# Performance work log

Measured on AMD Instinct MI355X. Metric: run time of the kernel, lower is better.

## Reference

```python
import jax, jax.numpy as jnp
import numpy as np

E = 4096      # num hyperedges (events)
H1 = 512      # hidden1
H2 = 128      # hidden2 (latent)
NA, NK, NV = 8192, 4096, 1024   # nodes per type: author / keyword / venue
NNZ = 131072  # nonzeros per incidence matrix
SCALE = 0.02  # weight init scale (keeps tanh/exp in sane range)


def setup_inputs() -> dict:
    key = jax.random.key(0)
    ks = iter(jax.random.split(key, 64))
    nrm = lambda shape, s=SCALE: jax.random.normal(next(ks), shape, jnp.float32) * s
    inp = {}
    for t, N in (("a", NA), ("k", NK), ("v", NV)):
        inp["rows_" + t] = jax.random.randint(next(ks), (NNZ,), 0, N, dtype=jnp.int32)
        inp["cols_" + t] = jax.random.randint(next(ks), (NNZ,), 0, E, dtype=jnp.int32)
        inp["vals_" + t] = jax.random.uniform(next(ks), (NNZ,), jnp.float32)
        inp["Wn_" + t] = nrm((E, H1));  inp["bn_" + t] = jnp.zeros((H1,), jnp.float32)
        inp["Wzm_" + t] = nrm((H1, H2)); inp["bzm_" + t] = jnp.zeros((H2,), jnp.float32)
        inp["Wzs_" + t] = nrm((H1, H2)); inp["bzs_" + t] = jnp.zeros((H2,), jnp.float32)
        inp["We_" + t] = nrm((N, H1));  inp["be_" + t] = jnp.zeros((H1,), jnp.float32)
        inp["eps_" + t] = jax.random.normal(next(ks), (N, H2), jnp.float32)
    inp["Watt"] = nrm((H1, H1 // 2)); inp["batt"] = jnp.zeros((H1 // 2,), jnp.float32)
    inp["uatt"] = nrm((H1 // 2,), 0.1)
    inp["Wem"] = nrm((H1, H2)); inp["bem"] = jnp.zeros((H2,), jnp.float32)
    inp["Wes"] = nrm((H1, H2)); inp["bes"] = jnp.zeros((H2,), jnp.float32)
    inp["eps_e"] = jax.random.normal(next(ks), (E, H2), jnp.float32)
    return inp


def _type_branch(rows, cols, vals, N, Wn, bn, Wzm, bzm, Wzs, bzs, We, be, eps):
    # node encoder: tanh(sparse_inc @ Wn + bn);  sparse_inc is [N, E] in COO form
    h = jnp.tanh(jax.ops.segment_sum(vals[:, None] * Wn[cols], rows, num_segments=N) + bn)
    zm = h @ Wzm + bzm
    zs = h @ Wzs + bzs
    z = zm + eps * jnp.exp(zs)          # reparameterization
    # edge encoder: tanh(sparse_inc^T @ We + be) -> [E, H1]
    e = jnp.tanh(jax.ops.segment_sum(vals[:, None] * We[rows], cols, num_segments=E) + be)
    return zm, z, e


def _forward(rows_a, cols_a, vals_a, Wn_a, bn_a, Wzm_a, bzm_a, Wzs_a, bzs_a, We_a, be_a, eps_a,
             rows_k, cols_k, vals_k, Wn_k, bn_k, Wzm_k, bzm_k, Wzs_k, bzs_k, We_k, be_k, eps_k,
             rows_v, cols_v, vals_v, Wn_v, bn_v, Wzm_v, bzm_v, Wzs_v, bzs_v, We_v, be_v, eps_v,
             Watt, batt, uatt, Wem, bem, Wes, bes, eps_e):
    zm_a, z_a, e_a = _type_branch(rows_a, cols_a, vals_a, NA, Wn_a, bn_a, Wzm_a, bzm_a, Wzs_a, bzs_a, We_a, be_a, eps_a)
    zm_k, z_k, e_k = _type_branch(rows_k, cols_k, vals_k, NK, Wn_k, bn_k, Wzm_k, bzm_k, Wzs_k, bzs_k, We_k, be_k, eps_k)
    zm_v, z_v, e_v = _type_branch(rows_v, cols_v, vals_v, NV, Wn_v, bn_v, Wzm_v, bzm_v, Wzs_v, bzs_v, We_v, be_v, eps_v)

    # HyperedgeAttention over node types: [E, T=3, H1]
    edge_embeds = jnp.stack([e_a, e_k, e_v], axis=1)
    u = jnp.tanh(jnp.einsum('eth,hd->etd', edge_embeds, Watt) + batt)
    scores = jnp.einsum('etd,d->et', u, uatt)
    alphas = jax.nn.softmax(scores, axis=1)                  # [E, T]
    edge_embed = jnp.einsum('et,eth->eh', alphas, edge_embeds)  # [E, H1]

    zem = edge_embed @ Wem + bem
    zes = edge_embed @ Wes + bes
    ze = zem + eps_e * jnp.exp(zes)

    # InnerDecoder: z_node @ z_edge^T per type, flattened (sampled and mean variants)
    recon = jnp.concatenate([
        (z_a @ ze.T).ravel(), (z_k @ ze.T).ravel(), (z_v @ ze.T).ravel(),
        (zm_a @ zem.T).ravel(), (zm_k @ zem.T).ravel(), (zm_v @ zem.T).ravel(),
    ])
    return recon


def reference(rows_a, cols_a, vals_a, rows_k, cols_k, vals_k, rows_v, cols_v, vals_v,
              Wn_a, bn_a, Wzm_a, bzm_a, Wzs_a, bzs_a, We_a, be_a, eps_a,
              Wn_k, bn_k, Wzm_k, bzm_k, Wzs_k, bzs_k, We_k, be_k, eps_k,
              Wn_v, bn_v, Wzm_v, bzm_v, Wzs_v, bzs_v, We_v, be_v, eps_v,
              Watt, batt, uatt, Wem, bem, Wes, bes, eps_e):
    return _forward(rows_a, cols_a, vals_a, Wn_a, bn_a, Wzm_a, bzm_a, Wzs_a, bzs_a, We_a, be_a, eps_a,
                    rows_k, cols_k, vals_k, Wn_k, bn_k, Wzm_k, bzm_k, Wzs_k, bzs_k, We_k, be_k, eps_k,
                    rows_v, cols_v, vals_v, Wn_v, bn_v, Wzm_v, bzm_v, Wzs_v, bzs_v, We_v, be_v, eps_v,
                    Watt, batt, uatt, Wem, bem, Wes, bes, eps_e)
```

## Files before the change

kernel.cpp:

```cpp
#include <hip/hip_runtime.h>
#include <hip/hip_bf16.h>

#define NE   4096
#define D1   512
#define D2   128
#define NNZV 131072
#define MTOT 13312

typedef __attribute__((ext_vector_type(8))) short bf16x8;
typedef __attribute__((ext_vector_type(4))) float f32x4;

struct Params {
  const int*   rows[3]; const int* cols[3]; const float* vals[3];
  const float* Wn[3];  const float* bn[3];
  const float* Wzm[3]; const float* bzm[3];
  const float* Wzs[3]; const float* bzs[3];
  const float* We[3];  const float* be[3];
  const float* eps[3];
  const float* Watt; const float* batt; const float* uatt;
  const float* Wem;  const float* bem;  const float* Wes; const float* bes;
  const float* eps_e;
  int* cnt[6]; int* ptr[6]; int* cur[6]; int2* spair[6];
  __hip_bfloat16* Wbf[6];
  __hip_bfloat16* hbf[3];
  __hip_bfloat16* ebf[3];
  __hip_bfloat16* eebf;
  __hip_bfloat16* Wzmt[3];
  __hip_bfloat16* Wzst[3];
  __hip_bfloat16* Wattt;
  __hip_bfloat16* Wemt;
  __hip_bfloat16* West;
  float* scores;
  __hip_bfloat16* Zbf; __hip_bfloat16* Zmbf; __hip_bfloat16* zebf; __hip_bfloat16* zembf;
  float* out;
  int rowbase[3];
  int n8pre[7];
  int ndw;
};

__device__ __forceinline__ float bf2f(short s) {
  return __uint_as_float((unsigned)(unsigned short)s << 16);
}

__device__ __forceinline__ int nseg_of(int sub) {
  if (sub & 1) return NE;
  int t = sub >> 1;
  return t == 0 ? 8192 : (t == 1 ? 4096 : 1024);
}

__global__ void prep_kernel(Params p) {
  int i = blockIdx.x * blockDim.x + threadIdx.x;
  if (i < p.ndw) { ((int*)p.cnt[0])[i] = 0; return; }
  int c = i - p.ndw;
  if (c < p.n8pre[6]) {
    int s = 0;
#pragma unroll
    for (int k = 1; k < 6; ++k) if (c >= p.n8pre[k]) s = k;
    int off8 = c - p.n8pre[s];
    int t = s >> 1;
    const float* src = (s & 1) ? p.We[t] : p.Wn[t];
    __hip_bfloat16* dst = p.Wbf[s];
    const float4 a = *(const float4*)&src[(size_t)off8 * 8];
    const float4 b = *(const float4*)&src[(size_t)off8 * 8 + 4];
    bf16x8 o;
    o[0] = (short)__bfloat16_as_ushort(__float2bfloat16(a.x));
    o[1] = (short)__bfloat16_as_ushort(__float2bfloat16(a.y));
    o[2] = (short)__bfloat16_as_ushort(__float2bfloat16(a.z));
    o[3] = (short)__bfloat16_as_ushort(__float2bfloat16(a.w));
    o[4] = (short)__bfloat16_as_ushort(__float2bfloat16(b.x));
    o[5] = (short)__bfloat16_as_ushort(__float2bfloat16(b.y));
    o[6] = (short)__bfloat16_as_ushort(__float2bfloat16(b.z));
    o[7] = (short)__bfloat16_as_ushort(__float2bfloat16(b.w));
    *(bf16x8*)&dst[(size_t)off8 * 8] = o;
    return;
  }
  int cz = c - p.n8pre[6];
  if (cz < 6 * D1 * D2) {
    int m = cz >> 16, e = cz & 65535;
    int t = m >> 1;
    const float* src = (m & 1) ? p.Wzs[t] : p.Wzm[t];
    __hip_bfloat16* dst = (m & 1) ? p.Wzst[t] : p.Wzmt[t];
    int k = e >> 7, n = e & 127;
    dst[n * D1 + k] = __float2bfloat16(src[e]);
    return;
  }
  int cz2 = cz - 6 * D1 * D2;
  if (cz2 < D1 * 256) {
    int k = cz2 >> 8, n = cz2 & 255;
    p.Wattt[n * D1 + k] = __float2bfloat16(p.Watt[(size_t)k * 256 + n]);
    return;
  }
  int cz3 = cz2 - D1 * 256;
  if (cz3 < 2 * D1 * D2) {
    int m = cz3 >> 16, e = cz3 & 65535;
    const float* src = m ? p.Wes : p.Wem;
    __hip_bfloat16* dst = m ? p.West : p.Wemt;
    int k = e >> 7, n = e & 127;
    dst[n * D1 + k] = __float2bfloat16(src[e]);
  }
}

__global__ void hist_kernel(Params p) {
  int i = blockIdx.x * blockDim.x + threadIdx.x;
  if (i >= 6 * NNZV) return;
  int sub = i >> 17, idx = i & (NNZV - 1);
  int type = sub >> 1, dir = sub & 1;
  int seg = dir ? p.cols[type][idx] : p.rows[type][idx];
  atomicAdd(&p.cnt[sub][seg], 1);
}

__global__ __launch_bounds__(1024) void scan_kernel(Params p) {
  int sub = blockIdx.x;
  int n = nseg_of(sub);
  const int* cnt = p.cnt[sub];
  int* ptr = p.ptr[sub];
  int* cur = p.cur[sub];
  __shared__ int lds[1024];
  int tid = threadIdx.x;
  int per = (n + 1023) >> 10;
  int base = tid * per;
  int s = 0;
  for (int q = 0; q < per; ++q) { int ix = base + q; if (ix < n) s += cnt[ix]; }
  lds[tid] = s;
  __syncthreads();
  for (int off = 1; off < 1024; off <<= 1) {
    int v = (tid >= off) ? lds[tid - off] : 0;
    __syncthreads();
    lds[tid] += v;
    __syncthreads();
  }
  int prefix = (tid == 0) ? 0 : lds[tid - 1];
  for (int q = 0; q < per; ++q) {
    int ix = base + q;
    if (ix < n) { int c = cnt[ix]; ptr[ix] = prefix; cur[ix] = prefix; prefix += c; }
  }
  if (tid == 1023) ptr[n] = lds[1023];
}

__global__ void scatter_kernel(Params p) {
  int i = blockIdx.x * blockDim.x + threadIdx.x;
  if (i >= 6 * NNZV) return;
  int sub = i >> 17, idx = i & (NNZV - 1);
  int type = sub >> 1, dir = sub & 1;
  int seg = dir ? p.cols[type][idx] : p.rows[type][idx];
  int oth = dir ? p.rows[type][idx] : p.cols[type][idx];
  int pos = atomicAdd(&p.cur[sub][seg], 1);
  p.spair[sub][pos] = make_int2(oth, __float_as_int(p.vals[type][idx]));
}

__global__ __launch_bounds__(128) void spmm_kernel(Params p) {
  int g = blockIdx.x * 2 + (threadIdx.x >> 6);
  int sub, seg;
  if      (g <  8192) { sub = 0; seg = g;         }
  else if (g < 12288) { sub = 1; seg = g - 8192;  }
  else if (g < 16384) { sub = 2; seg = g - 12288; }
  else if (g < 20480) { sub = 3; seg = g - 16384; }
  else if (g < 21504) { sub = 4; seg = g - 20480; }
  else                { sub = 5; seg = g - 21504; }
  int type = sub >> 1, dir = sub & 1;
  const __hip_bfloat16* W = p.Wbf[sub];
  const float* bias = dir ? p.be[type] : p.bn[type];
  const int*  ptr  = p.ptr[sub];
  const int2* pair = p.spair[sub];
  int lane = threadIdx.x & 63;
  int c0 = lane * 8;
  float acc[8];
#pragma unroll
  for (int j = 0; j < 8; ++j) acc[j] = 0.f;
  int q0 = ptr[seg], q1 = ptr[seg + 1];
  int q = q0;
  for (; q + 4 <= q1; q += 4) {
    int2 pr0 = pair[q], pr1 = pair[q + 1], pr2 = pair[q + 2], pr3 = pair[q + 3];
    const bf16x8 w0 = *(const bf16x8*)(W + (size_t)pr0.x * D1 + c0);
    const bf16x8 w1 = *(const bf16x8*)(W + (size_t)pr1.x * D1 + c0);
    const bf16x8 w2 = *(const bf16x8*)(W + (size_t)pr2.x * D1 + c0);
    const bf16x8 w3 = *(const bf16x8*)(W + (size_t)pr3.x * D1 + c0);
    float v0 = __int_as_float(pr0.y), v1 = __int_as_float(pr1.y);
    float v2 = __int_as_float(pr2.y), v3 = __int_as_float(pr3.y);
#pragma unroll
    for (int j = 0; j < 8; ++j)
      acc[j] += v0 * bf2f(w0[j]) + v1 * bf2f(w1[j]) + v2 * bf2f(w2[j]) + v3 * bf2f(w3[j]);
  }
  for (; q < q1; ++q) {
    int2 pr = pair[q];
    const bf16x8 wv = *(const bf16x8*)(W + (size_t)pr.x * D1 + c0);
    float v = __int_as_float(pr.y);
#pragma unroll
    for (int j = 0; j < 8; ++j) acc[j] += v * bf2f(wv[j]);
  }
  const float4 b0 = *(const float4*)&bias[c0];
  const float4 b1 = *(const float4*)&bias[c0 + 4];
  float r[8];
  r[0] = tanhf(acc[0] + b0.x); r[1] = tanhf(acc[1] + b0.y);
  r[2] = tanhf(acc[2] + b0.z); r[3] = tanhf(acc[3] + b0.w);
  r[4] = tanhf(acc[4] + b1.x); r[5] = tanhf(acc[5] + b1.y);
  r[6] = tanhf(acc[6] + b1.z); r[7] = tanhf(acc[7] + b1.w);
  bf16x8 ob;
#pragma unroll
  for (int j = 0; j < 8; ++j) ob[j] = (short)__bfloat16_as_ushort(__float2bfloat16(r[j]));
  __hip_bfloat16* outp = dir ? p.ebf[type] : p.hbf[type];
  *(bf16x8*)&outp[(size_t)seg * D1 + c0] = ob;
}

__global__ __launch_bounds__(256) void zmzs_scores_kernel(Params p) {
  int b = blockIdx.x;
  int wid = threadIdx.x >> 6, lane = threadIdx.x & 63;
  int rloc = lane & 15, kg = lane >> 4;
  f32x4 zero = {0.f, 0.f, 0.f, 0.f};
  if (b < 208) {
    int type, blk;
    if      (b < 128) { type = 0; blk = b;       }
    else if (b < 192) { type = 1; blk = b - 128; }
    else              { type = 2; blk = b - 192; }
    int row0 = blk * 64 + wid * 16;
    const __hip_bfloat16* A  = p.hbf[type];
    const __hip_bfloat16* Bm = p.Wzmt[type];
    const __hip_bfloat16* Bs = p.Wzst[type];
    int mrow = row0 + rloc;
    f32x4 accm[8], accs[8];
#pragma unroll
    for (int nf = 0; nf < 8; ++nf) { accm[nf] = zero; accs[nf] = zero; }
    for (int kk = 0; kk < 16; ++kk) {
      bf16x8 a = *(const bf16x8*)(A + (size_t)mrow * D1 + kk * 32 + kg * 8);
#pragma unroll
      for (int nf = 0; nf < 8; ++nf) {
        int ncol = nf * 16 + rloc;
        bf16x8 bm = *(const bf16x8*)(Bm + (size_t)ncol * D1 + kk * 32 + kg * 8);
        accm[nf] = __builtin_amdgcn_mfma_f32_16x16x32_bf16(a, bm, accm[nf], 0, 0, 0);
        bf16x8 bs = *(const bf16x8*)(Bs + (size_t)ncol * D1 + kk * 32 + kg * 8);
        accs[nf] = __builtin_amdgcn_mfma_f32_16x16x32_bf16(a, bs, accs[nf], 0, 0, 0);
      }
    }
    int base = p.rowbase[type];
    const float* eps = p.eps[type];
    const float* bzm = p.bzm[type];
    const float* bzs = p.bzs[type];
    int rbase = row0 + kg * 4;
#pragma unroll
    for (int nf = 0; nf < 8; ++nf) {
      int col = nf * 16 + rloc;
      float bm = bzm[col], bs = bzs[col];
#pragma unroll
      for (int jj = 0; jj < 4; ++jj) {
        int row = rbase + jj;
        float zm = accm[nf][jj] + bm;
        float zs = accs[nf][jj] + bs;
        float ep = eps[(size_t)row * D2 + col];
        float z  = zm + ep * expf(zs);
        size_t oi = (size_t)(base + row) * D2 + col;
        p.Zmbf[oi] = __float2bfloat16(zm);
        p.Zbf[oi]  = __float2bfloat16(z);
      }
    }
  } else {
    int wtile = (b - 208) * 4 + wid;
    int t = wtile >> 8;
    int tile = wtile & 255;
    const __hip_bfloat16* A = p.ebf[t];
    const __hip_bfloat16* B = p.Wattt;
    int mrow = tile * 16 + rloc;
    f32x4 acc[16];
#pragma unroll
    for (int nf = 0; nf < 16; ++nf) acc[nf] = zero;
    for (int kk = 0; kk < 16; ++kk) {
      bf16x8 a = *(const bf16x8*)(A + (size_t)mrow * D1 + kk * 32 + kg * 8);
#pragma unroll
      for (int nf = 0; nf < 16; ++nf) {
        int ncol = nf * 16 + rloc;
        bf16x8 bv = *(const bf16x8*)(B + (size_t)ncol * D1 + kk * 32 + kg * 8);
        acc[nf] = __builtin_amdgcn_mfma_f32_16x16x32_bf16(a, bv, acc[nf], 0, 0, 0);
      }
    }
    float part[4] = {0.f, 0.f, 0.f, 0.f};
#pragma unroll
    for (int nf = 0; nf < 16; ++nf) {
      int col = nf * 16 + rloc;
      float ua = p.uatt[col], ba = p.batt[col];
#pragma unroll
      for (int jj = 0; jj < 4; ++jj)
        part[jj] += ua * tanhf(acc[nf][jj] + ba);
    }
#pragma unroll
    for (int off = 1; off < 16; off <<= 1) {
#pragma unroll
      for (int jj = 0; jj < 4; ++jj)
        part[jj] += __shfl_xor(part[jj], off, 64);
    }
    if (rloc == 0) {
#pragma unroll
      for (int jj = 0; jj < 4; ++jj) {
        int e = tile * 16 + kg * 4 + jj;
        p.scores[e * 3 + t] = part[jj];
      }
    }
  }
}

__global__ __launch_bounds__(256) void combine_kernel(Params p) {
  int e = blockIdx.x * 4 + (threadIdx.x >> 6);
  int lane = threadIdx.x & 63;
  float s0 = p.scores[e * 3 + 0];
  float s1 = p.scores[e * 3 + 1];
  float s2 = p.scores[e * 3 + 2];
  float m = fmaxf(s0, fmaxf(s1, s2));
  float a0 = expf(s0 - m), a1 = expf(s1 - m), a2 = expf(s2 - m);
  float inv = 1.f / (a0 + a1 + a2);
  a0 *= inv; a1 *= inv; a2 *= inv;
  int c0 = lane * 8;
  const bf16x8 va = *(const bf16x8*)(p.ebf[0] + (size_t)e * D1 + c0);
  const bf16x8 vk = *(const bf16x8*)(p.ebf[1] + (size_t)e * D1 + c0);
  const bf16x8 vv = *(const bf16x8*)(p.ebf[2] + (size_t)e * D1 + c0);
  bf16x8 o;
#pragma unroll
  for (int j = 0; j < 8; ++j) {
    float v = a0 * bf2f(va[j]) + a1 * bf2f(vk[j]) + a2 * bf2f(vv[j]);
    o[j] = (short)__bfloat16_as_ushort(__float2bfloat16(v));
  }
  *(bf16x8*)&p.eebf[(size_t)e * D1 + c0] = o;
}

__global__ __launch_bounds__(256) void zemzs_kernel(Params p) {
  int wid = threadIdx.x >> 6, lane = threadIdx.x & 63;
  int rloc = lane & 15, kg = lane >> 4;
  int row0 = blockIdx.x * 32 + (wid >> 1) * 16;
  int nh = wid & 1;
  const __hip_bfloat16* A  = p.eebf;
  const __hip_bfloat16* Bm = p.Wemt;
  const __hip_bfloat16* Bs = p.West;
  int mrow = row0 + rloc;
  f32x4 accm[4], accs[4];
  f32x4 zero = {0.f, 0.f, 0.f, 0.f};
#pragma unroll
  for (int nf = 0; nf < 4; ++nf) { accm[nf] = zero; accs[nf] = zero; }
  for (int kk = 0; kk < 16; ++kk) {
    bf16x8 a = *(const bf16x8*)(A + (size_t)mrow * D1 + kk * 32 + kg * 8);
#pragma unroll
    for (int nf = 0; nf < 4; ++nf) {
      int ncol = nh * 64 + nf * 16 + rloc;
      bf16x8 bm = *(const bf16x8*)(Bm + (size_t)ncol * D1 + kk * 32 + kg * 8);
      accm[nf] = __builtin_amdgcn_mfma_f32_16x16x32_bf16(a, bm, accm[nf], 0, 0, 0);
      bf16x8 bs = *(const bf16x8*)(Bs + (size_t)ncol * D1 + kk * 32 + kg * 8);
      accs[nf] = __builtin_amdgcn_mfma_f32_16x16x32_bf16(a, bs, accs[nf], 0, 0, 0);
    }
  }
  int rbase = row0 + kg * 4;
#pragma unroll
  for (int nf = 0; nf < 4; ++nf) {
    int col = nh * 64 + nf * 16 + rloc;
    float bm = p.bem[col], bs = p.bes[col];
#pragma unroll
    for (int jj = 0; jj < 4; ++jj) {
      int row = rbase + jj;
      float zm = accm[nf][jj] + bm;
      float zs = accs[nf][jj] + bs;
      float ep = p.eps_e[(size_t)row * D2 + col];
      float z  = zm + ep * expf(zs);
      size_t oi = (size_t)row * D2 + col;
      p.zembf[oi] = __float2bfloat16(zm);
      p.zebf[oi]  = __float2bfloat16(z);
    }
  }
}

#define DT_N 128
__global__ __launch_bounds__(256) void decode_kernel(Params p) {
  __shared__ __align__(16) float cs[64][DT_N + 4];
  int which = blockIdx.z;
  const __hip_bfloat16* A = which ? p.Zmbf  : p.Zbf;
  const __hip_bfloat16* B = which ? p.zembf : p.zebf;
  float* C = p.out + (size_t)which * MTOT * NE;
  int n0 = blockIdx.x * DT_N;
  int m0 = blockIdx.y * 64;
  int wid  = threadIdx.x >> 6;
  int lane = threadIdx.x & 63;
  int rloc = lane & 15;
  int kg   = lane >> 4;
  int mrow = m0 + wid * 16 + rloc;
  bf16x8 a[4];
#pragma unroll
  for (int kk = 0; kk < 4; ++kk)
    a[kk] = *(const bf16x8*)(A + (size_t)mrow * D2 + kk * 32 + kg * 8);
  f32x4 acc[DT_N / 16];
  f32x4 zero = {0.f, 0.f, 0.f, 0.f};
#pragma unroll
  for (int nf = 0; nf < DT_N / 16; ++nf) acc[nf] = zero;
#pragma unroll
  for (int nf = 0; nf < DT_N / 16; ++nf) {
    int ncol = n0 + nf * 16 + rloc;
#pragma unroll
    for (int kk = 0; kk < 4; ++kk) {
      bf16x8 bv = *(const bf16x8*)(B + (size_t)ncol * D2 + kk * 32 + kg * 8);
      acc[nf] = __builtin_amdgcn_mfma_f32_16x16x32_bf16(a[kk], bv, acc[nf], 0, 0, 0);
    }
  }
#pragma unroll
  for (int nf = 0; nf < DT_N / 16; ++nf)
#pragma unroll
    for (int jj = 0; jj < 4; ++jj)
      cs[wid * 16 + kg * 4 + jj][nf * 16 + rloc] = acc[nf][jj];
  __syncthreads();
  int r_l  = threadIdx.x >> 5;
  int c4   = (threadIdx.x & 31) * 4;
#pragma unroll
  for (int it = 0; it < 8; ++it) {
    int r = it * 8 + r_l;
    f32x4 v = *(const f32x4*)&cs[r][c4];
    __builtin_nontemporal_store(v, (f32x4*)&C[(size_t)(m0 + r) * NE + n0 + c4]);
  }
}

extern "C" void kernel_launch(void* const* d_in, const int* in_sizes, int n_in,
                              void* d_out, int out_size, void* d_ws, size_t ws_size,
                              hipStream_t stream) {
  (void)in_sizes; (void)n_in; (void)out_size; (void)ws_size;
  static const int Ns[3] = {8192, 4096, 1024};
  static const int NsegH[6] = {8192, 4096, 4096, 4096, 1024, 4096};

  Params p;
  for (int t = 0; t < 3; ++t) {
    const int o = t * 12;
    p.rows[t] = (const int*)d_in[o + 0];
    p.cols[t] = (const int*)d_in[o + 1];
    p.vals[t] = (const float*)d_in[o + 2];
    p.Wn[t]   = (const float*)d_in[o + 3];
    p.bn[t]   = (const float*)d_in[o + 4];
    p.Wzm[t]  = (const float*)d_in[o + 5];
    p.bzm[t]  = (const float*)d_in[o + 6];
    p.Wzs[t]  = (const float*)d_in[o + 7];
    p.bzs[t]  = (const float*)d_in[o + 8];
    p.We[t]   = (const float*)d_in[o + 9];
    p.be[t]   = (const float*)d_in[o + 10];
    p.eps[t]  = (const float*)d_in[o + 11];
  }
  p.Watt  = (const float*)d_in[36];
  p.batt  = (const float*)d_in[37];
  p.uatt  = (const float*)d_in[38];
  p.Wem   = (const float*)d_in[39];
  p.bem   = (const float*)d_in[40];
  p.Wes   = (const float*)d_in[41];
  p.bes   = (const float*)d_in[42];
  p.eps_e = (const float*)d_in[43];
  p.out = (float*)d_out;
  p.rowbase[0] = 0; p.rowbase[1] = 8192; p.rowbase[2] = 12288;

  char* ws = (char*)d_ws;
  size_t off = 0;
  auto alloc = [&](size_t bytes) -> char* {
    char* r = ws + off;
    off += (bytes + 255) & ~(size_t)255;
    return r;
  };
  for (int s = 0; s < 6; ++s) p.cnt[s] = (int*)alloc((size_t)(NsegH[s] + 1) * 4);
  size_t cnt_bytes = off;
  for (int s = 0; s < 6; ++s) {
    p.ptr[s]   = (int*)alloc((size_t)(NsegH[s] + 1) * 4);
    p.cur[s]   = (int*)alloc((size_t)(NsegH[s] + 1) * 4);
    p.spair[s] = (int2*)alloc((size_t)NNZV * 8);
  }
  for (int s = 0; s < 6; ++s) {
    int t = s >> 1;
    int nrows = (s & 1) ? Ns[t] : NE;
    p.Wbf[s] = (__hip_bfloat16*)alloc((size_t)nrows * D1 * 2);
  }
  for (int t = 0; t < 3; ++t) p.hbf[t]  = (__hip_bfloat16*)alloc((size_t)Ns[t] * D1 * 2);
  for (int t = 0; t < 3; ++t) p.ebf[t]  = (__hip_bfloat16*)alloc((size_t)NE * D1 * 2);
  p.eebf = (__hip_bfloat16*)alloc((size_t)NE * D1 * 2);
  for (int t = 0; t < 3; ++t) p.Wzmt[t] = (__hip_bfloat16*)alloc((size_t)D2 * D1 * 2);
  for (int t = 0; t < 3; ++t) p.Wzst[t] = (__hip_bfloat16*)alloc((size_t)D2 * D1 * 2);
  p.Wattt = (__hip_bfloat16*)alloc((size_t)256 * D1 * 2);
  p.Wemt  = (__hip_bfloat16*)alloc((size_t)D2 * D1 * 2);
  p.West  = (__hip_bfloat16*)alloc((size_t)D2 * D1 * 2);
  p.scores = (float*)alloc((size_t)NE * 3 * 4);
  p.Zbf    = (__hip_bfloat16*)alloc((size_t)MTOT * D2 * 2);
  p.Zmbf   = (__hip_bfloat16*)alloc((size_t)MTOT * D2 * 2);
  p.zebf   = (__hip_bfloat16*)alloc((size_t)NE * D2 * 2);
  p.zembf  = (__hip_bfloat16*)alloc((size_t)NE * D2 * 2);

  p.ndw = (int)(cnt_bytes >> 2);
  p.n8pre[0] = 0;
  for (int s = 0; s < 6; ++s) {
    int t = s >> 1;
    int nrows = (s & 1) ? Ns[t] : NE;
    p.n8pre[s + 1] = p.n8pre[s] + nrows * (D1 / 8);
  }

  int prep_threads = p.ndw + p.n8pre[6] + 6 * D1 * D2 + D1 * 256 + 2 * D1 * D2;
  prep_kernel       <<<(prep_threads + 255) / 256, 256, 0, stream>>>(p);
  hist_kernel       <<<(6 * NNZV + 255) / 256, 256, 0, stream>>>(p);
  scan_kernel       <<<6, 1024, 0, stream>>>(p);
  scatter_kernel    <<<(6 * NNZV + 255) / 256, 256, 0, stream>>>(p);
  spmm_kernel       <<<12800, 128, 0, stream>>>(p);
  zmzs_scores_kernel<<<400, 256, 0, stream>>>(p);
  combine_kernel    <<<1024, 256, 0, stream>>>(p);
  zemzs_kernel      <<<128, 256, 0, stream>>>(p);
  decode_kernel     <<<dim3(NE / DT_N, 208, 2), 256, 0, stream>>>(p);
}
```

Baseline: 542.7 us.

## Fuse attention combine into zemzs GEMM and histogram into prep kernel

The softmax-weighted combine of the three edge embeddings now runs inside the zem/zes GEMM kernel. Each block builds its 32 combined rows in shared memory, so the eebf intermediate buffer and its global round trip go away. The histogram atomics move into the prep kernel, and a small zero kernel clears the counters beforehand, which removes one launch. The transposed weight conversions now iterate so that consecutive threads write contiguous destinations, which coalesces stores but strides the reads.

```diff
diff --git a/kernel.cpp b/kernel.cpp
--- a/kernel.cpp
+++ b/kernel.cpp
@@ -24,7 +24,6 @@
   __hip_bfloat16* Wbf[6];
   __hip_bfloat16* hbf[3];
   __hip_bfloat16* ebf[3];
-  __hip_bfloat16* eebf;
   __hip_bfloat16* Wzmt[3];
   __hip_bfloat16* Wzst[3];
   __hip_bfloat16* Wattt;
@@ -41,6 +40,9 @@
 __device__ __forceinline__ float bf2f(short s) {
   return __uint_as_float((unsigned)(unsigned short)s << 16);
 }
+__device__ __forceinline__ short f2bf(float f) {
+  return (short)__bfloat16_as_ushort(__float2bfloat16(f));
+}
 
 __device__ __forceinline__ int nseg_of(int sub) {
   if (sub & 1) return NE;
@@ -48,10 +50,21 @@
   return t == 0 ? 8192 : (t == 1 ? 4096 : 1024);
 }
 
+__global__ void zero_kernel(int* base, int ndw) {
+  int i = blockIdx.x * blockDim.x + threadIdx.x;
+  if (i < ndw) base[i] = 0;
+}
+
 __global__ void prep_kernel(Params p) {
   int i = blockIdx.x * blockDim.x + threadIdx.x;
-  if (i < p.ndw) { ((int*)p.cnt[0])[i] = 0; return; }
-  int c = i - p.ndw;
+  if (i < 6 * NNZV) {
+    int sub = i >> 17, idx = i & (NNZV - 1);
+    int type = sub >> 1, dir = sub & 1;
+    int seg = dir ? p.cols[type][idx] : p.rows[type][idx];
+    atomicAdd(&p.cnt[sub][seg], 1);
+    return;
+  }
+  int c = i - 6 * NNZV;
   if (c < p.n8pre[6]) {
     int s = 0;
 #pragma unroll
@@ -63,50 +76,35 @@
     const float4 a = *(const float4*)&src[(size_t)off8 * 8];
     const float4 b = *(const float4*)&src[(size_t)off8 * 8 + 4];
     bf16x8 o;
-    o[0] = (short)__bfloat16_as_ushort(__float2bfloat16(a.x));
-    o[1] = (short)__bfloat16_as_ushort(__float2bfloat16(a.y));
-    o[2] = (short)__bfloat16_as_ushort(__float2bfloat16(a.z));
-    o[3] = (short)__bfloat16_as_ushort(__float2bfloat16(a.w));
-    o[4] = (short)__bfloat16_as_ushort(__float2bfloat16(b.x));
-    o[5] = (short)__bfloat16_as_ushort(__float2bfloat16(b.y));
-    o[6] = (short)__bfloat16_as_ushort(__float2bfloat16(b.z));
-    o[7] = (short)__bfloat16_as_ushort(__float2bfloat16(b.w));
+    o[0] = f2bf(a.x); o[1] = f2bf(a.y); o[2] = f2bf(a.z); o[3] = f2bf(a.w);
+    o[4] = f2bf(b.x); o[5] = f2bf(b.y); o[6] = f2bf(b.z); o[7] = f2bf(b.w);
     *(bf16x8*)&dst[(size_t)off8 * 8] = o;
     return;
   }
   int cz = c - p.n8pre[6];
   if (cz < 6 * D1 * D2) {
-    int m = cz >> 16, e = cz & 65535;
+    int m = cz >> 16, e2 = cz & 65535;
     int t = m >> 1;
     const float* src = (m & 1) ? p.Wzs[t] : p.Wzm[t];
     __hip_bfloat16* dst = (m & 1) ? p.Wzst[t] : p.Wzmt[t];
-    int k = e >> 7, n = e & 127;
-    dst[n * D1 + k] = __float2bfloat16(src[e]);
+    int n = e2 >> 9, k = e2 & 511;
+    dst[n * D1 + k] = __float2bfloat16(src[(size_t)k * D2 + n]);
     return;
   }
   int cz2 = cz - 6 * D1 * D2;
   if (cz2 < D1 * 256) {
-    int k = cz2 >> 8, n = cz2 & 255;
+    int n = cz2 >> 9, k = cz2 & 511;
     p.Wattt[n * D1 + k] = __float2bfloat16(p.Watt[(size_t)k * 256 + n]);
     return;
   }
   int cz3 = cz2 - D1 * 256;
   if (cz3 < 2 * D1 * D2) {
-    int m = cz3 >> 16, e = cz3 & 65535;
+    int m = cz3 >> 16, e2 = cz3 & 65535;
     const float* src = m ? p.Wes : p.Wem;
     __hip_bfloat16* dst = m ? p.West : p.Wemt;
-    int k = e >> 7, n = e & 127;
-    dst[n * D1 + k] = __float2bfloat16(src[e]);
-  }
-}
-
-__global__ void hist_kernel(Params p) {
-  int i = blockIdx.x * blockDim.x + threadIdx.x;
-  if (i >= 6 * NNZV) return;
-  int sub = i >> 17, idx = i & (NNZV - 1);
-  int type = sub >> 1, dir = sub & 1;
-  int seg = dir ? p.cols[type][idx] : p.rows[type][idx];
-  atomicAdd(&p.cnt[sub][seg], 1);
+    int n = e2 >> 9, k = e2 & 511;
+    dst[n * D1 + k] = __float2bfloat16(src[(size_t)k * D2 + n]);
+  }
 }
 
 __global__ __launch_bounds__(1024) void scan_kernel(Params p) {
@@ -197,7 +195,7 @@
   r[6] = tanhf(acc[6] + b1.z); r[7] = tanhf(acc[7] + b1.w);
   bf16x8 ob;
 #pragma unroll
-  for (int j = 0; j < 8; ++j) ob[j] = (short)__bfloat16_as_ushort(__float2bfloat16(r[j]));
+  for (int j = 0; j < 8; ++j) ob[j] = f2bf(r[j]);
   __hip_bfloat16* outp = dir ? p.ebf[type] : p.hbf[type];
   *(bf16x8*)&outp[(size_t)seg * D1 + c0] = ob;
 }
@@ -296,44 +294,46 @@
   }
 }
 
-__global__ __launch_bounds__(256) void combine_kernel(Params p) {
-  int e = blockIdx.x * 4 + (threadIdx.x >> 6);
-  int lane = threadIdx.x & 63;
-  float s0 = p.scores[e * 3 + 0];
-  float s1 = p.scores[e * 3 + 1];
-  float s2 = p.scores[e * 3 + 2];
-  float m = fmaxf(s0, fmaxf(s1, s2));
-  float a0 = expf(s0 - m), a1 = expf(s1 - m), a2 = expf(s2 - m);
-  float inv = 1.f / (a0 + a1 + a2);
-  a0 *= inv; a1 *= inv; a2 *= inv;
-  int c0 = lane * 8;
-  const bf16x8 va = *(const bf16x8*)(p.ebf[0] + (size_t)e * D1 + c0);
-  const bf16x8 vk = *(const bf16x8*)(p.ebf[1] + (size_t)e * D1 + c0);
-  const bf16x8 vv = *(const bf16x8*)(p.ebf[2] + (size_t)e * D1 + c0);
-  bf16x8 o;
-#pragma unroll
-  for (int j = 0; j < 8; ++j) {
-    float v = a0 * bf2f(va[j]) + a1 * bf2f(vk[j]) + a2 * bf2f(vv[j]);
-    o[j] = (short)__bfloat16_as_ushort(__float2bfloat16(v));
-  }
-  *(bf16x8*)&p.eebf[(size_t)e * D1 + c0] = o;
-}
-
 __global__ __launch_bounds__(256) void zemzs_kernel(Params p) {
-  int wid = threadIdx.x >> 6, lane = threadIdx.x & 63;
+  __shared__ __align__(16) __hip_bfloat16 ee[32][D1 + 8];
+  int tid = threadIdx.x;
+  int row0 = blockIdx.x * 32;
+  {
+    int el = tid >> 3;
+    int e  = row0 + el;
+    int cc = (tid & 7) * 64;
+    float s0 = p.scores[e * 3 + 0];
+    float s1 = p.scores[e * 3 + 1];
+    float s2 = p.scores[e * 3 + 2];
+    float m = fmaxf(s0, fmaxf(s1, s2));
+    float a0 = expf(s0 - m), a1 = expf(s1 - m), a2 = expf(s2 - m);
+    float inv = 1.f / (a0 + a1 + a2);
+    a0 *= inv; a1 *= inv; a2 *= inv;
+#pragma unroll
+    for (int c8 = 0; c8 < 64; c8 += 8) {
+      const bf16x8 va = *(const bf16x8*)(p.ebf[0] + (size_t)e * D1 + cc + c8);
+      const bf16x8 vk = *(const bf16x8*)(p.ebf[1] + (size_t)e * D1 + cc + c8);
+      const bf16x8 vv = *(const bf16x8*)(p.ebf[2] + (size_t)e * D1 + cc + c8);
+      bf16x8 o;
+#pragma unroll
+      for (int j = 0; j < 8; ++j)
+        o[j] = f2bf(a0 * bf2f(va[j]) + a1 * bf2f(vk[j]) + a2 * bf2f(vv[j]));
+      *(bf16x8*)&ee[el][cc + c8] = o;
+    }
+  }
+  __syncthreads();
+  int wid = tid >> 6, lane = tid & 63;
   int rloc = lane & 15, kg = lane >> 4;
-  int row0 = blockIdx.x * 32 + (wid >> 1) * 16;
+  int rowl = (wid >> 1) * 16 + rloc;
   int nh = wid & 1;
-  const __hip_bfloat16* A  = p.eebf;
   const __hip_bfloat16* Bm = p.Wemt;
   const __hip_bfloat16* Bs = p.West;
-  int mrow = row0 + rloc;
   f32x4 accm[4], accs[4];
   f32x4 zero = {0.f, 0.f, 0.f, 0.f};
 #pragma unroll
   for (int nf = 0; nf < 4; ++nf) { accm[nf] = zero; accs[nf] = zero; }
   for (int kk = 0; kk < 16; ++kk) {
-    bf16x8 a = *(const bf16x8*)(A + (size_t)mrow * D1 + kk * 32 + kg * 8);
+    bf16x8 a = *(const bf16x8*)&ee[rowl][kk * 32 + kg * 8];
 #pragma unroll
     for (int nf = 0; nf < 4; ++nf) {
       int ncol = nh * 64 + nf * 16 + rloc;
@@ -343,7 +343,7 @@
       accs[nf] = __builtin_amdgcn_mfma_f32_16x16x32_bf16(a, bs, accs[nf], 0, 0, 0);
     }
   }
-  int rbase = row0 + kg * 4;
+  int rbase = row0 + (wid >> 1) * 16 + kg * 4;
 #pragma unroll
   for (int nf = 0; nf < 4; ++nf) {
     int col = nh * 64 + nf * 16 + rloc;
@@ -464,7 +464,6 @@
   }
   for (int t = 0; t < 3; ++t) p.hbf[t]  = (__hip_bfloat16*)alloc((size_t)Ns[t] * D1 * 2);
   for (int t = 0; t < 3; ++t) p.ebf[t]  = (__hip_bfloat16*)alloc((size_t)NE * D1 * 2);
-  p.eebf = (__hip_bfloat16*)alloc((size_t)NE * D1 * 2);
   for (int t = 0; t < 3; ++t) p.Wzmt[t] = (__hip_bfloat16*)alloc((size_t)D2 * D1 * 2);
   for (int t = 0; t < 3; ++t) p.Wzst[t] = (__hip_bfloat16*)alloc((size_t)D2 * D1 * 2);
   p.Wattt = (__hip_bfloat16*)alloc((size_t)256 * D1 * 2);
@@ -484,14 +483,13 @@
     p.n8pre[s + 1] = p.n8pre[s] + nrows * (D1 / 8);
   }
 
-  int prep_threads = p.ndw + p.n8pre[6] + 6 * D1 * D2 + D1 * 256 + 2 * D1 * D2;
+  int prep_threads = 6 * NNZV + p.n8pre[6] + 6 * D1 * D2 + D1 * 256 + 2 * D1 * D2;
+  zero_kernel       <<<(p.ndw + 255) / 256, 256, 0, stream>>>((int*)d_ws, p.ndw);
   prep_kernel       <<<(prep_threads + 255) / 256, 256, 0, stream>>>(p);
-  hist_kernel       <<<(6 * NNZV + 255) / 256, 256, 0, stream>>>(p);
   scan_kernel       <<<6, 1024, 0, stream>>>(p);
   scatter_kernel    <<<(6 * NNZV + 255) / 256, 256, 0, stream>>>(p);
   spmm_kernel       <<<12800, 128, 0, stream>>>(p);
   zmzs_scores_kernel<<<400, 256, 0, stream>>>(p);
-  combine_kernel    <<<1024, 256, 0, stream>>>(p);
   zemzs_kernel      <<<128, 256, 0, stream>>>(p);
   decode_kernel     <<<dim3(NE / DT_N, 208, 2), 256, 0, stream>>>(p);
 }
```

Measured after the change: 552.1 us. No clear change (+1.7%).

## Restructure decode as persistent kernel writing full 16-row output stripes

Applied to the files above, without the earlier changes.

The decode GEMM becomes a persistent kernel with 208 blocks. Each block loops over 16-row chunks of the stacked node latents and writes complete 4096-column rows in four 1024-column passes through a larger shared-memory staging buffer, replacing the old 64x128 tile grid. The aim is long contiguous nontemporal stores into the large fp32 output and lower launch/tile overhead. In exchange each chunk has a serial compute-sync-store pattern with two barriers and no overlap, plus higher register and LDS use, which may reduce occupancy. A small bf16 conversion helper is also added as a cleanup.

```diff
diff --git a/kernel.cpp b/kernel.cpp
--- a/kernel.cpp
+++ b/kernel.cpp
@@ -41,6 +41,9 @@
 __device__ __forceinline__ float bf2f(short s) {
   return __uint_as_float((unsigned)(unsigned short)s << 16);
 }
+__device__ __forceinline__ short f2bf(float f) {
+  return (short)__bfloat16_as_ushort(__float2bfloat16(f));
+}
 
 __device__ __forceinline__ int nseg_of(int sub) {
   if (sub & 1) return NE;
@@ -63,14 +66,8 @@
     const float4 a = *(const float4*)&src[(size_t)off8 * 8];
     const float4 b = *(const float4*)&src[(size_t)off8 * 8 + 4];
     bf16x8 o;
-    o[0] = (short)__bfloat16_as_ushort(__float2bfloat16(a.x));
-    o[1] = (short)__bfloat16_as_ushort(__float2bfloat16(a.y));
-    o[2] = (short)__bfloat16_as_ushort(__float2bfloat16(a.z));
-    o[3] = (short)__bfloat16_as_ushort(__float2bfloat16(a.w));
-    o[4] = (short)__bfloat16_as_ushort(__float2bfloat16(b.x));
-    o[5] = (short)__bfloat16_as_ushort(__float2bfloat16(b.y));
-    o[6] = (short)__bfloat16_as_ushort(__float2bfloat16(b.z));
-    o[7] = (short)__bfloat16_as_ushort(__float2bfloat16(b.w));
+    o[0] = f2bf(a.x); o[1] = f2bf(a.y); o[2] = f2bf(a.z); o[3] = f2bf(a.w);
+    o[4] = f2bf(b.x); o[5] = f2bf(b.y); o[6] = f2bf(b.z); o[7] = f2bf(b.w);
     *(bf16x8*)&dst[(size_t)off8 * 8] = o;
     return;
   }
@@ -197,7 +194,7 @@
   r[6] = tanhf(acc[6] + b1.z); r[7] = tanhf(acc[7] + b1.w);
   bf16x8 ob;
 #pragma unroll
-  for (int j = 0; j < 8; ++j) ob[j] = (short)__bfloat16_as_ushort(__float2bfloat16(r[j]));
+  for (int j = 0; j < 8; ++j) ob[j] = f2bf(r[j]);
   __hip_bfloat16* outp = dir ? p.ebf[type] : p.hbf[type];
   *(bf16x8*)&outp[(size_t)seg * D1 + c0] = ob;
 }
@@ -314,7 +311,7 @@
 #pragma unroll
   for (int j = 0; j < 8; ++j) {
     float v = a0 * bf2f(va[j]) + a1 * bf2f(vk[j]) + a2 * bf2f(vv[j]);
-    o[j] = (short)__bfloat16_as_ushort(__float2bfloat16(v));
+    o[j] = f2bf(v);
   }
   *(bf16x8*)&p.eebf[(size_t)e * D1 + c0] = o;
 }
@@ -362,50 +359,51 @@
   }
 }
 
-#define DT_N 128
 __global__ __launch_bounds__(256) void decode_kernel(Params p) {
-  __shared__ __align__(16) float cs[64][DT_N + 4];
-  int which = blockIdx.z;
-  const __hip_bfloat16* A = which ? p.Zmbf  : p.Zbf;
-  const __hip_bfloat16* B = which ? p.zembf : p.zebf;
-  float* C = p.out + (size_t)which * MTOT * NE;
-  int n0 = blockIdx.x * DT_N;
-  int m0 = blockIdx.y * 64;
+  __shared__ __align__(16) float cs[16][1024];
   int wid  = threadIdx.x >> 6;
   int lane = threadIdx.x & 63;
   int rloc = lane & 15;
   int kg   = lane >> 4;
-  int mrow = m0 + wid * 16 + rloc;
-  bf16x8 a[4];
-#pragma unroll
-  for (int kk = 0; kk < 4; ++kk)
-    a[kk] = *(const bf16x8*)(A + (size_t)mrow * D2 + kk * 32 + kg * 8);
-  f32x4 acc[DT_N / 16];
   f32x4 zero = {0.f, 0.f, 0.f, 0.f};
-#pragma unroll
-  for (int nf = 0; nf < DT_N / 16; ++nf) acc[nf] = zero;
-#pragma unroll
-  for (int nf = 0; nf < DT_N / 16; ++nf) {
-    int ncol = n0 + nf * 16 + rloc;
-#pragma unroll
-    for (int kk = 0; kk < 4; ++kk) {
-      bf16x8 bv = *(const bf16x8*)(B + (size_t)ncol * D2 + kk * 32 + kg * 8);
-      acc[nf] = __builtin_amdgcn_mfma_f32_16x16x32_bf16(a[kk], bv, acc[nf], 0, 0, 0);
-    }
-  }
-#pragma unroll
-  for (int nf = 0; nf < DT_N / 16; ++nf)
-#pragma unroll
-    for (int jj = 0; jj < 4; ++jj)
-      cs[wid * 16 + kg * 4 + jj][nf * 16 + rloc] = acc[nf][jj];
-  __syncthreads();
-  int r_l  = threadIdx.x >> 5;
-  int c4   = (threadIdx.x & 31) * 4;
-#pragma unroll
-  for (int it = 0; it < 8; ++it) {
-    int r = it * 8 + r_l;
-    f32x4 v = *(const f32x4*)&cs[r][c4];
-    __builtin_nontemporal_store(v, (f32x4*)&C[(size_t)(m0 + r) * NE + n0 + c4]);
+  for (int c = blockIdx.x; c < 1664; c += 208) {
+    int which = c >= 832;
+    int row0 = (which ? c - 832 : c) * 16;
+    const __hip_bfloat16* A = which ? p.Zmbf  : p.Zbf;
+    const __hip_bfloat16* B = which ? p.zembf : p.zebf;
+    float* C = p.out + (size_t)which * MTOT * NE;
+    int mrow = row0 + rloc;
+    bf16x8 a[4];
+#pragma unroll
+    for (int kk = 0; kk < 4; ++kk)
+      a[kk] = *(const bf16x8*)(A + (size_t)mrow * D2 + kk * 32 + kg * 8);
+    for (int cp = 0; cp < 4; ++cp) {
+      f32x4 acc[16];
+#pragma unroll
+      for (int nf = 0; nf < 16; ++nf) acc[nf] = zero;
+#pragma unroll
+      for (int nf = 0; nf < 16; ++nf) {
+        int ncol = cp * 1024 + wid * 256 + nf * 16 + rloc;
+#pragma unroll
+        for (int kk = 0; kk < 4; ++kk) {
+          bf16x8 bv = *(const bf16x8*)(B + (size_t)ncol * D2 + kk * 32 + kg * 8);
+          acc[nf] = __builtin_amdgcn_mfma_f32_16x16x32_bf16(a[kk], bv, acc[nf], 0, 0, 0);
+        }
+      }
+#pragma unroll
+      for (int nf = 0; nf < 16; ++nf)
+#pragma unroll
+        for (int jj = 0; jj < 4; ++jj)
+          cs[kg * 4 + jj][wid * 256 + nf * 16 + rloc] = acc[nf][jj];
+      __syncthreads();
+#pragma unroll
+      for (int it = 0; it < 16; ++it) {
+        f32x4 v = *(const f32x4*)&cs[it][threadIdx.x * 4];
+        __builtin_nontemporal_store(v,
+          (f32x4*)&C[(size_t)(row0 + it) * NE + cp * 1024 + threadIdx.x * 4]);
+      }
+      __syncthreads();
+    }
   }
 }
 
@@ -493,5 +491,5 @@
   zmzs_scores_kernel<<<400, 256, 0, stream>>>(p);
   combine_kernel    <<<1024, 256, 0, stream>>>(p);
   zemzs_kernel      <<<128, 256, 0, stream>>>(p);
-  decode_kernel     <<<dim3(NE / DT_N, 208, 2), 256, 0, stream>>>(p);
-}
+  decode_kernel     <<<208, 256, 0, stream>>>(p);
+}
```

New measurement: 591.2 us. 1.09x slower.
